# Optimization experiments

Measured on AMD Instinct MI355X. Metric: run time of the kernel, lower is better.

Reference implementation:

```python
import jax, jax.numpy as jnp
import numpy as np

N_NODES = 100000
N_EDGES = 1600000
DIM_IN = 128
DIM_OUT = 128


def setup_inputs() -> dict:
    key = jax.random.key(0)
    k1, k2, k3 = jax.random.split(key, 3)
    x = jax.random.normal(k1, (N_NODES, DIM_IN), dtype=jnp.float32)
    W = jax.random.normal(k2, (DIM_OUT, DIM_IN), dtype=jnp.float32) * (1.0 / np.sqrt(DIM_IN))
    bias = jnp.zeros((DIM_OUT,), dtype=jnp.float32)
    edge_index = jax.random.randint(k3, (2, N_EDGES), 0, N_NODES, dtype=jnp.int64)
    return {"x": x, "W": W, "bias": bias, "edge_index": edge_index}


def reference(x, W, bias, edge_index):
    N = x.shape[0]
    # add self loops
    loops = jnp.arange(N, dtype=edge_index.dtype)
    row = jnp.concatenate([edge_index[0], loops])  # source nodes (x_j)
    col = jnp.concatenate([edge_index[1], loops])  # target nodes (aggregation)
    # linear transform (no bias inside lin)
    h = x @ W.T  # [N, out]
    # symmetric degree normalization, degree computed over col incl. self loops
    deg = jax.ops.segment_sum(jnp.ones_like(col, dtype=x.dtype), col, num_segments=N)
    deg_inv_sqrt = jnp.where(deg > 0, deg ** -0.5, 0.0)
    norm = deg_inv_sqrt[row] * deg_inv_sqrt[col]  # [E+N]
    # gather-scale-scatter_add
    msg = norm[:, None] * h[row]  # [E+N, out]
    out = jax.ops.segment_sum(msg, col, num_segments=N)
    return out + bias
```

## Files before the change

kernel.cpp:

```cpp
#include <hip/hip_runtime.h>

#define DIM 128
#define CAP 64
#define BUCKET_BLOCKS 2048
#define GEMM_BLOCKS 1563


typedef __attribute__((ext_vector_type(8))) short bf16x8;
typedef __attribute__((ext_vector_type(4))) float f32x4;
typedef __attribute__((ext_vector_type(4))) int i32x4;

__device__ __forceinline__ unsigned short f2bf(float f) {
  unsigned int u = __float_as_uint(f);
  return (unsigned short)((u + 0x7FFFu + ((u >> 16) & 1u)) >> 16);
}
__device__ __forceinline__ float bf2f(unsigned int s) {
  return __uint_as_float(s << 16);
}

__global__ __launch_bounds__(256) void prep_kernel(
    const float* __restrict__ W, unsigned short* __restrict__ Wb,
    int* __restrict__ cnt, int N) {
  int i = blockIdx.x * 256 + threadIdx.x;
  if (i < DIM * DIM) Wb[i] = f2bf(W[i]);
  if (i < N) cnt[i] = 0;
}

__global__ __launch_bounds__(256) void bucket_kernel(
    const int* __restrict__ rows, const int* __restrict__ cols,
    int* __restrict__ cnt, int* __restrict__ csr, int E, int N) {
  int bid = blockIdx.x;
  int g = bid & 7;
  int gblk = bid >> 3;
  int lo = (int)((long long)g * N / 8);
  int hi = (int)((long long)(g + 1) * N / 8);
  const i32x4* cols4 = (const i32x4*)cols;
  const i32x4* rows4 = (const i32x4*)rows;
  int E4 = E >> 2;
  for (int i = gblk * 256 + threadIdx.x; i < E4;
       i += (BUCKET_BLOCKS / 8) * 256) {
    i32x4 c4 = __builtin_nontemporal_load(&cols4[i]);
    bool mx = (c4.x >= lo) & (c4.x < hi);
    bool my = (c4.y >= lo) & (c4.y < hi);
    bool mz = (c4.z >= lo) & (c4.z < hi);
    bool mw = (c4.w >= lo) & (c4.w < hi);
    if (mx | my | mz | mw) {
      i32x4 r4 = __builtin_nontemporal_load(&rows4[i]);
      if (mx) {
        int k = atomicAdd(&cnt[c4.x], 1);
        if (k < CAP) csr[(size_t)c4.x * CAP + k] = r4.x;
      }
      if (my) {
        int k = atomicAdd(&cnt[c4.y], 1);
        if (k < CAP) csr[(size_t)c4.y * CAP + k] = r4.y;
      }
      if (mz) {
        int k = atomicAdd(&cnt[c4.z], 1);
        if (k < CAP) csr[(size_t)c4.z * CAP + k] = r4.z;
      }
      if (mw) {
        int k = atomicAdd(&cnt[c4.w], 1);
        if (k < CAP) csr[(size_t)c4.w * CAP + k] = r4.w;
      }
    }
  }
  if (bid < 8 && gblk == 0) {
    for (int e = (E & ~3) + threadIdx.x; e < E; e += 256) {
      int c = cols[e];
      if (c >= lo && c < hi) {
        int k = atomicAdd(&cnt[c], 1);
        if (k < CAP) csr[(size_t)c * CAP + k] = rows[e];
      }
    }
  }
}

__global__ __launch_bounds__(256) void gemm_kernel(
    const float* __restrict__ x, const unsigned short* __restrict__ Wb,
    unsigned short* __restrict__ h, int N) {
  int wid = blockIdx.x * 4 + (threadIdx.x >> 6);
  int m0 = wid * 16;
  if (m0 >= N) return;
  int lane = threadIdx.x & 63;
  int mr = lane & 15;
  int quad = lane >> 4;

  bf16x8 afrag[4];
  const float* xrow = x + (size_t)(m0 + mr) * DIM + quad * 8;
#pragma unroll
  for (int ks = 0; ks < 4; ++ks) {
    f32x4 lo = __builtin_nontemporal_load((const f32x4*)(xrow + ks * 32));
    f32x4 hi = __builtin_nontemporal_load((const f32x4*)(xrow + ks * 32 + 4));
    bf16x8 a;
    a[0] = (short)f2bf(lo.x); a[1] = (short)f2bf(lo.y);
    a[2] = (short)f2bf(lo.z); a[3] = (short)f2bf(lo.w);
    a[4] = (short)f2bf(hi.x); a[5] = (short)f2bf(hi.y);
    a[6] = (short)f2bf(hi.z); a[7] = (short)f2bf(hi.w);
    afrag[ks] = a;
  }

#pragma unroll
  for (int nt = 0; nt < 8; ++nt) {
    f32x4 c = {0.f, 0.f, 0.f, 0.f};
#pragma unroll
    for (int ks = 0; ks < 4; ++ks) {
      bf16x8 b = *(const bf16x8*)(Wb + (size_t)(nt * 16 + mr) * DIM +
                                  ks * 32 + quad * 8);
      c = __builtin_amdgcn_mfma_f32_16x16x32_bf16(afrag[ks], b, c, 0, 0, 0);
    }
#pragma unroll
    for (int r = 0; r < 4; ++r) {
      h[(size_t)(m0 + quad * 4 + r) * DIM + nt * 16 + mr] = f2bf(c[r]);
    }
  }
}

__global__ __launch_bounds__(256) void gather_kernel(
    const uint4* __restrict__ h4, const int* __restrict__ csr,
    const int* __restrict__ cnt, const float4* __restrict__ bias4,
    float* __restrict__ out, int N) {
  int node = blockIdx.x * 16 + (threadIdx.x >> 4);
  if (node >= N) return;
  int lane = threadIdx.x & 15;

  int degN = cnt[node];
  float dn = rsqrtf((float)degN + 1.0f);
  int deg = degN > CAP ? CAP : degN;
  const int* seg = csr + (size_t)node * CAP;

  float acc[8];
  {
    uint4 s = h4[(size_t)node * 16 + lane];
    acc[0] = dn * bf2f(s.x & 0xFFFF); acc[1] = dn * bf2f(s.x >> 16);
    acc[2] = dn * bf2f(s.y & 0xFFFF); acc[3] = dn * bf2f(s.y >> 16);
    acc[4] = dn * bf2f(s.z & 0xFFFF); acc[5] = dn * bf2f(s.z >> 16);
    acc[6] = dn * bf2f(s.w & 0xFFFF); acc[7] = dn * bf2f(s.w >> 16);
  }
  int j = 0;
  for (; j + 2 <= deg; j += 2) {
    int r0 = __builtin_nontemporal_load(seg + j);
    int r1 = __builtin_nontemporal_load(seg + j + 1);
    uint4 v0 = h4[(size_t)r0 * 16 + lane];
    uint4 v1 = h4[(size_t)r1 * 16 + lane];
    float dr0 = rsqrtf((float)cnt[r0] + 1.0f);
    float dr1 = rsqrtf((float)cnt[r1] + 1.0f);
    acc[0] += dr0 * bf2f(v0.x & 0xFFFF); acc[1] += dr0 * bf2f(v0.x >> 16);
    acc[2] += dr0 * bf2f(v0.y & 0xFFFF); acc[3] += dr0 * bf2f(v0.y >> 16);
    acc[4] += dr0 * bf2f(v0.z & 0xFFFF); acc[5] += dr0 * bf2f(v0.z >> 16);
    acc[6] += dr0 * bf2f(v0.w & 0xFFFF); acc[7] += dr0 * bf2f(v0.w >> 16);
    acc[0] += dr1 * bf2f(v1.x & 0xFFFF); acc[1] += dr1 * bf2f(v1.x >> 16);
    acc[2] += dr1 * bf2f(v1.y & 0xFFFF); acc[3] += dr1 * bf2f(v1.y >> 16);
    acc[4] += dr1 * bf2f(v1.z & 0xFFFF); acc[5] += dr1 * bf2f(v1.z >> 16);
    acc[6] += dr1 * bf2f(v1.w & 0xFFFF); acc[7] += dr1 * bf2f(v1.w >> 16);
  }
  if (j < deg) {
    int r = __builtin_nontemporal_load(seg + j);
    uint4 v = h4[(size_t)r * 16 + lane];
    float dr = rsqrtf((float)cnt[r] + 1.0f);
    acc[0] += dr * bf2f(v.x & 0xFFFF); acc[1] += dr * bf2f(v.x >> 16);
    acc[2] += dr * bf2f(v.y & 0xFFFF); acc[3] += dr * bf2f(v.y >> 16);
    acc[4] += dr * bf2f(v.z & 0xFFFF); acc[5] += dr * bf2f(v.z >> 16);
    acc[6] += dr * bf2f(v.w & 0xFFFF); acc[7] += dr * bf2f(v.w >> 16);
  }
  float4 bA = bias4[lane * 2], bB = bias4[lane * 2 + 1];
  f32x4 oA = {dn * acc[0] + bA.x, dn * acc[1] + bA.y,
              dn * acc[2] + bA.z, dn * acc[3] + bA.w};
  f32x4 oB = {dn * acc[4] + bB.x, dn * acc[5] + bB.y,
              dn * acc[6] + bB.z, dn * acc[7] + bB.w};
  f32x4* outv = (f32x4*)out;
  __builtin_nontemporal_store(oA, &outv[(size_t)node * 32 + lane * 2]);
  __builtin_nontemporal_store(oB, &outv[(size_t)node * 32 + lane * 2 + 1]);
}

extern "C" void kernel_launch(void* const* d_in, const int* in_sizes, int n_in,
                              void* d_out, int out_size, void* d_ws, size_t ws_size,
                              hipStream_t stream) {
  const float* x    = (const float*)d_in[0];
  const float* W    = (const float*)d_in[1];
  const float* bias = (const float*)d_in[2];
  const int*   ei   = (const int*)d_in[3];

  const int N = in_sizes[0] / DIM;
  const int E = in_sizes[3] / 2;
  const int* rows = ei;
  const int* cols = ei + E;
  float* out = (float*)d_out;
  char* ws = (char*)d_ws;

  int* cnt = (int*)ws;
  unsigned short* Wb = (unsigned short*)(ws + 409600);
  int* csr = (int*)(ws + 442368);
  unsigned short* h = (unsigned short*)(ws + 26042368);

  prep_kernel<<<(N + 255) / 256, 256, 0, stream>>>(W, Wb, cnt, N);
  bucket_kernel<<<BUCKET_BLOCKS, 256, 0, stream>>>(rows, cols, cnt, csr, E, N);
  gemm_kernel<<<GEMM_BLOCKS, 256, 0, stream>>>(x, Wb, h, N);
  gather_kernel<<<(N + 15) / 16, 256, 0, stream>>>(
      (const uint4*)h, csr, cnt, (const float4*)bias, out, N);
}
```

Measured before the change: 287.6 us.

## Slice h into column-major 16-wide panels and prescale by source degree in GEMM

```diff
diff --git a/kernel.cpp b/kernel.cpp
--- a/kernel.cpp
+++ b/kernel.cpp
@@ -39,13 +39,13 @@
   int E4 = E >> 2;
   for (int i = gblk * 256 + threadIdx.x; i < E4;
        i += (BUCKET_BLOCKS / 8) * 256) {
-    i32x4 c4 = __builtin_nontemporal_load(&cols4[i]);
+    i32x4 c4 = cols4[i];
     bool mx = (c4.x >= lo) & (c4.x < hi);
     bool my = (c4.y >= lo) & (c4.y < hi);
     bool mz = (c4.z >= lo) & (c4.z < hi);
     bool mw = (c4.w >= lo) & (c4.w < hi);
     if (mx | my | mz | mw) {
-      i32x4 r4 = __builtin_nontemporal_load(&rows4[i]);
+      i32x4 r4 = rows4[i];
       if (mx) {
         int k = atomicAdd(&cnt[c4.x], 1);
         if (k < CAP) csr[(size_t)c4.x * CAP + k] = r4.x;
@@ -64,7 +64,7 @@
       }
     }
   }
-  if (bid < 8 && gblk == 0) {
+  if (bid < 8) {
     for (int e = (E & ~3) + threadIdx.x; e < E; e += 256) {
       int c = cols[e];
       if (c >= lo && c < hi) {
@@ -77,7 +77,7 @@
 
 __global__ __launch_bounds__(256) void gemm_kernel(
     const float* __restrict__ x, const unsigned short* __restrict__ Wb,
-    unsigned short* __restrict__ h, int N) {
+    const int* __restrict__ cnt, unsigned short* __restrict__ h, int N) {
   int wid = blockIdx.x * 4 + (threadIdx.x >> 6);
   int m0 = wid * 16;
   if (m0 >= N) return;
@@ -99,6 +99,11 @@
     afrag[ks] = a;
   }
 
+  float drr[4];
+#pragma unroll
+  for (int r = 0; r < 4; ++r)
+    drr[r] = rsqrtf((float)cnt[m0 + quad * 4 + r] + 1.0f);
+
 #pragma unroll
   for (int nt = 0; nt < 8; ++nt) {
     f32x4 c = {0.f, 0.f, 0.f, 0.f};
@@ -110,66 +115,59 @@
     }
 #pragma unroll
     for (int r = 0; r < 4; ++r) {
-      h[(size_t)(m0 + quad * 4 + r) * DIM + nt * 16 + mr] = f2bf(c[r]);
+      h[((size_t)nt * N + (m0 + quad * 4 + r)) * 16 + mr] = f2bf(drr[r] * c[r]);
     }
   }
 }
 
 __global__ __launch_bounds__(256) void gather_kernel(
-    const uint4* __restrict__ h4, const int* __restrict__ csr,
-    const int* __restrict__ cnt, const float4* __restrict__ bias4,
-    float* __restrict__ out, int N) {
-  int node = blockIdx.x * 16 + (threadIdx.x >> 4);
+    const unsigned short* __restrict__ h,
+    const int* __restrict__ csr, const int* __restrict__ cnt,
+    const float4* __restrict__ bias4, float* __restrict__ out, int N) {
+  int s = blockIdx.x & 7;
+  int node = (blockIdx.x >> 3) * 64 + (threadIdx.x >> 2);
   if (node >= N) return;
-  int lane = threadIdx.x & 15;
+  int sub = threadIdx.x & 3;
+  int pair = sub >> 1;
+  int half = sub & 1;
 
+  const unsigned short* hs = h + (size_t)s * N * 16 + half * 8;
   int degN = cnt[node];
   float dn = rsqrtf((float)degN + 1.0f);
   int deg = degN > CAP ? CAP : degN;
   const int* seg = csr + (size_t)node * CAP;
 
-  float acc[8];
-  {
-    uint4 s = h4[(size_t)node * 16 + lane];
-    acc[0] = dn * bf2f(s.x & 0xFFFF); acc[1] = dn * bf2f(s.x >> 16);
-    acc[2] = dn * bf2f(s.y & 0xFFFF); acc[3] = dn * bf2f(s.y >> 16);
-    acc[4] = dn * bf2f(s.z & 0xFFFF); acc[5] = dn * bf2f(s.z >> 16);
-    acc[6] = dn * bf2f(s.w & 0xFFFF); acc[7] = dn * bf2f(s.w >> 16);
+  float acc[8] = {0.f, 0.f, 0.f, 0.f, 0.f, 0.f, 0.f, 0.f};
+  if (pair == 0) {
+    uint4 v = *(const uint4*)(hs + (size_t)node * 16);
+    acc[0] = bf2f(v.x & 0xFFFF); acc[1] = bf2f(v.x >> 16);
+    acc[2] = bf2f(v.y & 0xFFFF); acc[3] = bf2f(v.y >> 16);
+    acc[4] = bf2f(v.z & 0xFFFF); acc[5] = bf2f(v.z >> 16);
+    acc[6] = bf2f(v.w & 0xFFFF); acc[7] = bf2f(v.w >> 16);
   }
-  int j = 0;
-  for (; j + 2 <= deg; j += 2) {
-    int r0 = __builtin_nontemporal_load(seg + j);
-    int r1 = __builtin_nontemporal_load(seg + j + 1);
-    uint4 v0 = h4[(size_t)r0 * 16 + lane];
-    uint4 v1 = h4[(size_t)r1 * 16 + lane];
-    float dr0 = rsqrtf((float)cnt[r0] + 1.0f);
-    float dr1 = rsqrtf((float)cnt[r1] + 1.0f);
-    acc[0] += dr0 * bf2f(v0.x & 0xFFFF); acc[1] += dr0 * bf2f(v0.x >> 16);
-    acc[2] += dr0 * bf2f(v0.y & 0xFFFF); acc[3] += dr0 * bf2f(v0.y >> 16);
-    acc[4] += dr0 * bf2f(v0.z & 0xFFFF); acc[5] += dr0 * bf2f(v0.z >> 16);
-    acc[6] += dr0 * bf2f(v0.w & 0xFFFF); acc[7] += dr0 * bf2f(v0.w >> 16);
-    acc[0] += dr1 * bf2f(v1.x & 0xFFFF); acc[1] += dr1 * bf2f(v1.x >> 16);
-    acc[2] += dr1 * bf2f(v1.y & 0xFFFF); acc[3] += dr1 * bf2f(v1.y >> 16);
-    acc[4] += dr1 * bf2f(v1.z & 0xFFFF); acc[5] += dr1 * bf2f(v1.z >> 16);
-    acc[6] += dr1 * bf2f(v1.w & 0xFFFF); acc[7] += dr1 * bf2f(v1.w >> 16);
+  for (int j = pair; j < deg; j += 2) {
+    int r = seg[j];
+    uint4 v = *(const uint4*)(hs + (size_t)r * 16);
+    acc[0] += bf2f(v.x & 0xFFFF); acc[1] += bf2f(v.x >> 16);
+    acc[2] += bf2f(v.y & 0xFFFF); acc[3] += bf2f(v.y >> 16);
+    acc[4] += bf2f(v.z & 0xFFFF); acc[5] += bf2f(v.z >> 16);
+    acc[6] += bf2f(v.w & 0xFFFF); acc[7] += bf2f(v.w >> 16);
   }
-  if (j < deg) {
-    int r = __builtin_nontemporal_load(seg + j);
-    uint4 v = h4[(size_t)r * 16 + lane];
-    float dr = rsqrtf((float)cnt[r] + 1.0f);
-    acc[0] += dr * bf2f(v.x & 0xFFFF); acc[1] += dr * bf2f(v.x >> 16);
-    acc[2] += dr * bf2f(v.y & 0xFFFF); acc[3] += dr * bf2f(v.y >> 16);
-    acc[4] += dr * bf2f(v.z & 0xFFFF); acc[5] += dr * bf2f(v.z >> 16);
-    acc[6] += dr * bf2f(v.w & 0xFFFF); acc[7] += dr * bf2f(v.w >> 16);
+#pragma unroll
+  for (int i = 0; i < 8; ++i) acc[i] += __shfl_xor(acc[i], 2);
+
+  if (pair == 0) {
+    float4 bA = bias4[s * 4 + half * 2];
+    float4 bB = bias4[s * 4 + half * 2 + 1];
+    f32x4 oA = {dn * acc[0] + bA.x, dn * acc[1] + bA.y,
+                dn * acc[2] + bA.z, dn * acc[3] + bA.w};
+    f32x4 oB = {dn * acc[4] + bB.x, dn * acc[5] + bB.y,
+                dn * acc[6] + bB.z, dn * acc[7] + bB.w};
+    f32x4* outv = (f32x4*)out;
+    size_t o = (size_t)node * 32 + s * 4 + half * 2;
+    __builtin_nontemporal_store(oA, &outv[o]);
+    __builtin_nontemporal_store(oB, &outv[o + 1]);
   }
-  float4 bA = bias4[lane * 2], bB = bias4[lane * 2 + 1];
-  f32x4 oA = {dn * acc[0] + bA.x, dn * acc[1] + bA.y,
-              dn * acc[2] + bA.z, dn * acc[3] + bA.w};
-  f32x4 oB = {dn * acc[4] + bB.x, dn * acc[5] + bB.y,
-              dn * acc[6] + bB.z, dn * acc[7] + bB.w};
-  f32x4* outv = (f32x4*)out;
-  __builtin_nontemporal_store(oA, &outv[(size_t)node * 32 + lane * 2]);
-  __builtin_nontemporal_store(oB, &outv[(size_t)node * 32 + lane * 2 + 1]);
 }
 
 extern "C" void kernel_launch(void* const* d_in, const int* in_sizes, int n_in,
@@ -194,7 +192,8 @@
 
   prep_kernel<<<(N + 255) / 256, 256, 0, stream>>>(W, Wb, cnt, N);
   bucket_kernel<<<BUCKET_BLOCKS, 256, 0, stream>>>(rows, cols, cnt, csr, E, N);
-  gemm_kernel<<<GEMM_BLOCKS, 256, 0, stream>>>(x, Wb, h, N);
-  gather_kernel<<<(N + 15) / 16, 256, 0, stream>>>(
-      (const uint4*)h, csr, cnt, (const float4*)bias, out, N);
+  gemm_kernel<<<GEMM_BLOCKS, 256, 0, stream>>>(x, Wb, cnt, h, N);
+  int chunks = (N + 63) / 64;
+  gather_kernel<<<chunks * 8, 256, 0, stream>>>(
+      h, csr, cnt, (const float4*)bias, out, N);
 }
```

Result: slower. 323.4 us (+12.4%).

## Fuse bucket and GEMM into one launch, unroll gather by four

Applied to the files above, without the earlier changes.

```diff
diff --git a/kernel.cpp b/kernel.cpp
--- a/kernel.cpp
+++ b/kernel.cpp
@@ -2,8 +2,9 @@
 
 #define DIM 128
 #define CAP 64
-#define BUCKET_BLOCKS 2048
-#define GEMM_BLOCKS 1563
+#define BUCKET_BLOCKS 1024
+#define GEMM_BLOCKS 1568
+#define GRID_COMBO (BUCKET_BLOCKS + GEMM_BLOCKS)
 
 
 typedef __attribute__((ext_vector_type(8))) short bf16x8;
@@ -16,6 +17,12 @@
 }
 __device__ __forceinline__ float bf2f(unsigned int s) {
   return __uint_as_float(s << 16);
+}
+__device__ __forceinline__ void add8(float* a, uint4 v, float s) {
+  a[0] += s * bf2f(v.x & 0xFFFF); a[1] += s * bf2f(v.x >> 16);
+  a[2] += s * bf2f(v.y & 0xFFFF); a[3] += s * bf2f(v.y >> 16);
+  a[4] += s * bf2f(v.z & 0xFFFF); a[5] += s * bf2f(v.z >> 16);
+  a[6] += s * bf2f(v.w & 0xFFFF); a[7] += s * bf2f(v.w >> 16);
 }
 
 __global__ __launch_bounds__(256) void prep_kernel(
@@ -26,91 +33,91 @@
   if (i < N) cnt[i] = 0;
 }
 
-__global__ __launch_bounds__(256) void bucket_kernel(
+__global__ __launch_bounds__(256) void combo_kernel(
     const int* __restrict__ rows, const int* __restrict__ cols,
-    int* __restrict__ cnt, int* __restrict__ csr, int E, int N) {
-  int bid = blockIdx.x;
-  int g = bid & 7;
-  int gblk = bid >> 3;
-  int lo = (int)((long long)g * N / 8);
-  int hi = (int)((long long)(g + 1) * N / 8);
-  const i32x4* cols4 = (const i32x4*)cols;
-  const i32x4* rows4 = (const i32x4*)rows;
-  int E4 = E >> 2;
-  for (int i = gblk * 256 + threadIdx.x; i < E4;
-       i += (BUCKET_BLOCKS / 8) * 256) {
-    i32x4 c4 = __builtin_nontemporal_load(&cols4[i]);
-    bool mx = (c4.x >= lo) & (c4.x < hi);
-    bool my = (c4.y >= lo) & (c4.y < hi);
-    bool mz = (c4.z >= lo) & (c4.z < hi);
-    bool mw = (c4.w >= lo) & (c4.w < hi);
-    if (mx | my | mz | mw) {
-      i32x4 r4 = __builtin_nontemporal_load(&rows4[i]);
-      if (mx) {
-        int k = atomicAdd(&cnt[c4.x], 1);
-        if (k < CAP) csr[(size_t)c4.x * CAP + k] = r4.x;
-      }
-      if (my) {
-        int k = atomicAdd(&cnt[c4.y], 1);
-        if (k < CAP) csr[(size_t)c4.y * CAP + k] = r4.y;
-      }
-      if (mz) {
-        int k = atomicAdd(&cnt[c4.z], 1);
-        if (k < CAP) csr[(size_t)c4.z * CAP + k] = r4.z;
-      }
-      if (mw) {
-        int k = atomicAdd(&cnt[c4.w], 1);
-        if (k < CAP) csr[(size_t)c4.w * CAP + k] = r4.w;
-      }
-    }
-  }
-  if (bid < 8 && gblk == 0) {
-    for (int e = (E & ~3) + threadIdx.x; e < E; e += 256) {
-      int c = cols[e];
-      if (c >= lo && c < hi) {
-        int k = atomicAdd(&cnt[c], 1);
-        if (k < CAP) csr[(size_t)c * CAP + k] = rows[e];
-      }
-    }
-  }
-}
-
-__global__ __launch_bounds__(256) void gemm_kernel(
+    int* __restrict__ cnt, int* __restrict__ csr,
     const float* __restrict__ x, const unsigned short* __restrict__ Wb,
-    unsigned short* __restrict__ h, int N) {
-  int wid = blockIdx.x * 4 + (threadIdx.x >> 6);
-  int m0 = wid * 16;
-  if (m0 >= N) return;
-  int lane = threadIdx.x & 63;
-  int mr = lane & 15;
-  int quad = lane >> 4;
-
-  bf16x8 afrag[4];
-  const float* xrow = x + (size_t)(m0 + mr) * DIM + quad * 8;
-#pragma unroll
-  for (int ks = 0; ks < 4; ++ks) {
-    f32x4 lo = __builtin_nontemporal_load((const f32x4*)(xrow + ks * 32));
-    f32x4 hi = __builtin_nontemporal_load((const f32x4*)(xrow + ks * 32 + 4));
-    bf16x8 a;
-    a[0] = (short)f2bf(lo.x); a[1] = (short)f2bf(lo.y);
-    a[2] = (short)f2bf(lo.z); a[3] = (short)f2bf(lo.w);
-    a[4] = (short)f2bf(hi.x); a[5] = (short)f2bf(hi.y);
-    a[6] = (short)f2bf(hi.z); a[7] = (short)f2bf(hi.w);
-    afrag[ks] = a;
-  }
-
-#pragma unroll
-  for (int nt = 0; nt < 8; ++nt) {
-    f32x4 c = {0.f, 0.f, 0.f, 0.f};
+    unsigned short* __restrict__ h, int E, int N) {
+  if (blockIdx.x < BUCKET_BLOCKS) {
+    int bid = blockIdx.x;
+    int g = bid & 7;
+    int gblk = bid >> 3;
+    int lo = (int)((long long)g * N / 8);
+    int hi = (int)((long long)(g + 1) * N / 8);
+    const i32x4* cols4 = (const i32x4*)cols;
+    const i32x4* rows4 = (const i32x4*)rows;
+    int E4 = E >> 2;
+    for (int i = gblk * 256 + threadIdx.x; i < E4;
+         i += (BUCKET_BLOCKS / 8) * 256) {
+      i32x4 c4 = cols4[i];
+      bool mx = (c4.x >= lo) & (c4.x < hi);
+      bool my = (c4.y >= lo) & (c4.y < hi);
+      bool mz = (c4.z >= lo) & (c4.z < hi);
+      bool mw = (c4.w >= lo) & (c4.w < hi);
+      if (mx | my | mz | mw) {
+        i32x4 r4 = rows4[i];
+        if (mx) {
+          int k = atomicAdd(&cnt[c4.x], 1);
+          if (k < CAP) csr[(size_t)c4.x * CAP + k] = r4.x;
+        }
+        if (my) {
+          int k = atomicAdd(&cnt[c4.y], 1);
+          if (k < CAP) csr[(size_t)c4.y * CAP + k] = r4.y;
+        }
+        if (mz) {
+          int k = atomicAdd(&cnt[c4.z], 1);
+          if (k < CAP) csr[(size_t)c4.z * CAP + k] = r4.z;
+        }
+        if (mw) {
+          int k = atomicAdd(&cnt[c4.w], 1);
+          if (k < CAP) csr[(size_t)c4.w * CAP + k] = r4.w;
+        }
+      }
+    }
+    if (gblk == 0) {
+      for (int e = (E & ~3) + threadIdx.x; e < E; e += 256) {
+        int c = cols[e];
+        if (c >= lo && c < hi) {
+          int k = atomicAdd(&cnt[c], 1);
+          if (k < CAP) csr[(size_t)c * CAP + k] = rows[e];
+        }
+      }
+    }
+  } else {
+    int wid = (blockIdx.x - BUCKET_BLOCKS) * 4 + (threadIdx.x >> 6);
+    int m0 = wid * 16;
+    if (m0 >= N) return;
+    int lane = threadIdx.x & 63;
+    int mr = lane & 15;
+    int quad = lane >> 4;
+
+    bf16x8 afrag[4];
+    const float* xrow = x + (size_t)(m0 + mr) * DIM + quad * 8;
 #pragma unroll
     for (int ks = 0; ks < 4; ++ks) {
-      bf16x8 b = *(const bf16x8*)(Wb + (size_t)(nt * 16 + mr) * DIM +
-                                  ks * 32 + quad * 8);
-      c = __builtin_amdgcn_mfma_f32_16x16x32_bf16(afrag[ks], b, c, 0, 0, 0);
-    }
-#pragma unroll
-    for (int r = 0; r < 4; ++r) {
-      h[(size_t)(m0 + quad * 4 + r) * DIM + nt * 16 + mr] = f2bf(c[r]);
+      float4 lo = *(const float4*)(xrow + ks * 32);
+      float4 hi = *(const float4*)(xrow + ks * 32 + 4);
+      bf16x8 a;
+      a[0] = (short)f2bf(lo.x); a[1] = (short)f2bf(lo.y);
+      a[2] = (short)f2bf(lo.z); a[3] = (short)f2bf(lo.w);
+      a[4] = (short)f2bf(hi.x); a[5] = (short)f2bf(hi.y);
+      a[6] = (short)f2bf(hi.z); a[7] = (short)f2bf(hi.w);
+      afrag[ks] = a;
+    }
+
+#pragma unroll
+    for (int nt = 0; nt < 8; ++nt) {
+      f32x4 c = {0.f, 0.f, 0.f, 0.f};
+#pragma unroll
+      for (int ks = 0; ks < 4; ++ks) {
+        bf16x8 b = *(const bf16x8*)(Wb + (size_t)(nt * 16 + mr) * DIM +
+                                    ks * 32 + quad * 8);
+        c = __builtin_amdgcn_mfma_f32_16x16x32_bf16(afrag[ks], b, c, 0, 0, 0);
+      }
+#pragma unroll
+      for (int r = 0; r < 4; ++r) {
+        h[(size_t)(m0 + quad * 4 + r) * DIM + nt * 16 + mr] = f2bf(c[r]);
+      }
     }
   }
 }
@@ -137,30 +144,26 @@
     acc[6] = dn * bf2f(s.w & 0xFFFF); acc[7] = dn * bf2f(s.w >> 16);
   }
   int j = 0;
-  for (; j + 2 <= deg; j += 2) {
-    int r0 = __builtin_nontemporal_load(seg + j);
-    int r1 = __builtin_nontemporal_load(seg + j + 1);
-    uint4 v0 = h4[(size_t)r0 * 16 + lane];
-    uint4 v1 = h4[(size_t)r1 * 16 + lane];
-    float dr0 = rsqrtf((float)cnt[r0] + 1.0f);
-    float dr1 = rsqrtf((float)cnt[r1] + 1.0f);
-    acc[0] += dr0 * bf2f(v0.x & 0xFFFF); acc[1] += dr0 * bf2f(v0.x >> 16);
-    acc[2] += dr0 * bf2f(v0.y & 0xFFFF); acc[3] += dr0 * bf2f(v0.y >> 16);
-    acc[4] += dr0 * bf2f(v0.z & 0xFFFF); acc[5] += dr0 * bf2f(v0.z >> 16);
-    acc[6] += dr0 * bf2f(v0.w & 0xFFFF); acc[7] += dr0 * bf2f(v0.w >> 16);
-    acc[0] += dr1 * bf2f(v1.x & 0xFFFF); acc[1] += dr1 * bf2f(v1.x >> 16);
-    acc[2] += dr1 * bf2f(v1.y & 0xFFFF); acc[3] += dr1 * bf2f(v1.y >> 16);
-    acc[4] += dr1 * bf2f(v1.z & 0xFFFF); acc[5] += dr1 * bf2f(v1.z >> 16);
-    acc[6] += dr1 * bf2f(v1.w & 0xFFFF); acc[7] += dr1 * bf2f(v1.w >> 16);
-  }
-  if (j < deg) {
+  for (; j + 4 <= deg; j += 4) {
+    i32x4 r4 = __builtin_nontemporal_load((const i32x4*)(seg + j));
+    uint4 v0 = h4[(size_t)r4.x * 16 + lane];
+    uint4 v1 = h4[(size_t)r4.y * 16 + lane];
+    uint4 v2 = h4[(size_t)r4.z * 16 + lane];
+    uint4 v3 = h4[(size_t)r4.w * 16 + lane];
+    float d0 = rsqrtf((float)cnt[r4.x] + 1.0f);
+    float d1 = rsqrtf((float)cnt[r4.y] + 1.0f);
+    float d2 = rsqrtf((float)cnt[r4.z] + 1.0f);
+    float d3 = rsqrtf((float)cnt[r4.w] + 1.0f);
+    add8(acc, v0, d0);
+    add8(acc, v1, d1);
+    add8(acc, v2, d2);
+    add8(acc, v3, d3);
+  }
+  for (; j < deg; ++j) {
     int r = __builtin_nontemporal_load(seg + j);
     uint4 v = h4[(size_t)r * 16 + lane];
     float dr = rsqrtf((float)cnt[r] + 1.0f);
-    acc[0] += dr * bf2f(v.x & 0xFFFF); acc[1] += dr * bf2f(v.x >> 16);
-    acc[2] += dr * bf2f(v.y & 0xFFFF); acc[3] += dr * bf2f(v.y >> 16);
-    acc[4] += dr * bf2f(v.z & 0xFFFF); acc[5] += dr * bf2f(v.z >> 16);
-    acc[6] += dr * bf2f(v.w & 0xFFFF); acc[7] += dr * bf2f(v.w >> 16);
+    add8(acc, v, dr);
   }
   float4 bA = bias4[lane * 2], bB = bias4[lane * 2 + 1];
   f32x4 oA = {dn * acc[0] + bA.x, dn * acc[1] + bA.y,
@@ -193,8 +196,8 @@
   unsigned short* h = (unsigned short*)(ws + 26042368);
 
   prep_kernel<<<(N + 255) / 256, 256, 0, stream>>>(W, Wb, cnt, N);
-  bucket_kernel<<<BUCKET_BLOCKS, 256, 0, stream>>>(rows, cols, cnt, csr, E, N);
-  gemm_kernel<<<GEMM_BLOCKS, 256, 0, stream>>>(x, Wb, h, N);
+  combo_kernel<<<GRID_COMBO, 256, 0, stream>>>(rows, cols, cnt, csr, x, Wb, h,
+                                               E, N);
   gather_kernel<<<(N + 15) / 16, 256, 0, stream>>>(
-      (const uint4*)h, csr, cnt, (const float4*)bias, out, N);
-}
+      (const uint4*)h, csr, cnt, (const float4*)bias, (float*)out, N);
+}
```

After: 266.5 us. 7.3% less time.
